# Performance work log

Hardware: AMD Instinct MI355X
Metric: run time of the kernel (lower is better)

## Reference

```python
import jax, jax.numpy as jnp
import numpy as np
import math

B, N, D, H = 1, 128, 256, 8
DK = D // H

def setup_inputs() -> dict:
    key = jax.random.key(0)
    ks = jax.random.split(key, 8)
    query = jax.random.normal(ks[0], (B, N, N, D), dtype=jnp.float32)
    key_t = jax.random.normal(ks[1], (B, N, N, D), dtype=jnp.float32)
    value = jax.random.normal(ks[2], (B, N, N, D), dtype=jnp.float32)
    mask = jax.random.randint(ks[3], (B, N, N, N), 0, 2).astype(jnp.bool_)
    s = 1.0 / math.sqrt(D)
    # torch nn.Linear weights: [out_features, in_features]
    Wk = jax.random.uniform(ks[4], (D, D), dtype=jnp.float32, minval=-s, maxval=s)
    Wv = jax.random.uniform(ks[5], (D, D), dtype=jnp.float32, minval=-s, maxval=s)
    Wq = jax.random.uniform(ks[6], (D, D), dtype=jnp.float32, minval=-s, maxval=s)
    Wo = jax.random.uniform(ks[7], (D, D), dtype=jnp.float32, minval=-s, maxval=s)
    return {"query": query, "key": key_t, "value": value, "mask": mask,
            "Wq": Wq, "Wk": Wk, "Wv": Wv, "Wo": Wo}

def reference(query, key, value, mask, Wq, Wk, Wv, Wo):
    b, n = query.shape[0], query.shape[1]
    # linear projections (no bias), then split heads -> [b, n, n, h, d_k]
    q = (query @ Wq.T).reshape(b, n, n, H, DK)
    k = (key @ Wk.T).reshape(b, n, n, H, DK)
    v = (value @ Wv.T).reshape(b, n, n, H, DK)
    scale = 1.0 / math.sqrt(DK)
    neg = jnp.float32(-1e9)
    m = mask[..., None]  # [b, n, n, n, 1] broadcast over heads
    # row attention: edge (x,y) attends over edges (x,z)
    scores_r = jnp.einsum('bxyhd,bxzhd->bxyzh', q, k) * scale
    scores_r = jnp.where(m, neg, scores_r)
    # column attention: edge (x,y) attends over edges (z,y)
    scores_l = jnp.einsum('bxyhd,bzyhd->bxyzh', q, k) * scale
    scores_l = jnp.where(m, neg, scores_l)
    scores = jnp.concatenate((scores_r, scores_l), axis=3)  # [b,n,n,2n,h]
    att = jax.nn.softmax(scores, axis=3)
    att_r, att_l = att[:, :, :, :n], att[:, :, :, n:]
    x_r = jnp.einsum('bxyzh,bxzhd->bxyhd', att_r, v)
    x_l = jnp.einsum('bxyzh,bzyhd->bxyhd', att_l, v)
    x = (x_r + x_l).reshape(b, n, n, D)
    return x @ Wo.T
```

## Files before the change

### kernel.cpp

```cpp
#include <hip/hip_runtime.h>
#include <hip/hip_bf16.h>
#include <math.h>

#define N_DIM 128
#define NH 8
#define DKH 32
#define M_ROWS (N_DIM * N_DIM)

typedef __attribute__((ext_vector_type(8))) short bf16x8;
typedef __attribute__((ext_vector_type(4))) float f32x4;

__device__ inline ushort f2b(float x) {
    union { __hip_bfloat16 b; ushort u; } c;
    c.b = __float2bfloat16(x);
    return c.u;
}

#define GLDS(src, dst) \
    __builtin_amdgcn_global_load_lds((const __attribute__((address_space(1))) void*)(src), \
                                     (__attribute__((address_space(3))) void*)(dst), 16, 0, 0)

__global__ __launch_bounds__(256) void cvt_w_kernel(const float* __restrict__ w0,
                                                    const float* __restrict__ w1,
                                                    const float* __restrict__ w2,
                                                    const float* __restrict__ w3,
                                                    ushort* __restrict__ out) {
    const int b = blockIdx.x;
    const int m = b >> 6;
    const float* src = (m == 0) ? w0 : (m == 1) ? w1 : (m == 2) ? w2 : w3;
    const int off = (b & 63) * 1024 + threadIdx.x * 4;
    float4 v = *(const float4*)(src + off);
    union { ushort u[4]; short4 s4; } p;
    p.u[0] = f2b(v.x); p.u[1] = f2b(v.y); p.u[2] = f2b(v.z); p.u[3] = f2b(v.w);
    *(short4*)(out + (size_t)m * 65536 + off) = p.s4;
}

template <bool ABF16, bool OBF16>
__global__ __launch_bounds__(512) void gemm_mfma(const void* __restrict__ Ain,
                                                 const ushort* __restrict__ Wb,
                                                 void* __restrict__ Cout) {
    __shared__ ushort As[2][64 * 32];
    __shared__ ushort Ws[2][256 * 32];
    const int tid = threadIdx.x;
    const int row0 = blockIdx.x * 64;
    const int w = tid >> 6, lane = tid & 63;
    const int lr = lane & 15, g = lane >> 4;
    const int wm = w & 3, wn = w >> 2;

    auto stage = [&](int t, int buf) {
        const int kbase = t * 32;
#pragma unroll
        for (int i = 0; i < 2; i++) {
            int c = i * 8 + w;
            const ushort* src = Wb + (size_t)(c * 16 + (lane >> 2)) * 256 + kbase + (lane & 3) * 8;
            GLDS(src, &Ws[buf][c * 512]);
        }
        if (ABF16) {
            if (tid < 256) {
                const ushort* Ab = (const ushort*)Ain;
                const ushort* src = Ab + (size_t)(row0 + w * 16 + (lane >> 2)) * 256 + kbase + (lane & 3) * 8;
                GLDS(src, &As[buf][w * 512]);
            }
        } else {
            const float* Af = (const float*)Ain;
            const int r = tid >> 3, k0 = (tid & 7) * 4;
            float4 v = *(const float4*)(Af + (size_t)(row0 + r) * 256 + kbase + k0);
            union { ushort u[4]; short4 s4; } p;
            p.u[0] = f2b(v.x); p.u[1] = f2b(v.y); p.u[2] = f2b(v.z); p.u[3] = f2b(v.w);
            *(short4*)&As[buf][r * 32 + k0] = p.s4;
        }
    };

    f32x4 acc[8];
    const f32x4 zero = {0.f, 0.f, 0.f, 0.f};
#pragma unroll
    for (int fc = 0; fc < 8; fc++) acc[fc] = zero;

    stage(0, 0);
    __syncthreads();

#pragma unroll
    for (int t = 0; t < 8; t++) {
        const int cur = t & 1;
        if (t < 7) stage(t + 1, cur ^ 1);
        bf16x8 aq = *(const bf16x8*)&As[cur][(wm * 16 + lr) * 32 + g * 8];
#pragma unroll
        for (int fc = 0; fc < 8; fc++) {
            bf16x8 bw = *(const bf16x8*)&Ws[cur][(wn * 128 + fc * 16 + lr) * 32 + g * 8];
            acc[fc] = __builtin_amdgcn_mfma_f32_16x16x32_bf16(aq, bw, acc[fc], 0, 0, 0);
        }
        __syncthreads();
    }

#pragma unroll
    for (int fc = 0; fc < 8; fc++) {
#pragma unroll
        for (int j = 0; j < 4; j++) {
            const int row = row0 + wm * 16 + g * 4 + j;
            const int col = wn * 128 + fc * 16 + lr;
            if (OBF16) ((ushort*)Cout)[(size_t)row * 256 + col] = f2b(acc[fc][j]);
            else       ((float*)Cout)[(size_t)row * 256 + col] = acc[fc][j];
        }
    }
}

template <int PASS>
__global__ __launch_bounds__(256) void attn_pass(const ushort* __restrict__ qb,
                                                 const ushort* __restrict__ kb,
                                                 const ushort* __restrict__ vb,
                                                 const int* __restrict__ mask,
                                                 float* __restrict__ ml,
                                                 float* __restrict__ sl,
                                                 float* __restrict__ Pl,
                                                 ushort* __restrict__ xb) {
    __shared__ ushort Qs[128 * 32];
    __shared__ ushort Ks[128 * 32];
    __shared__ ushort Vt[32 * 128];
    __shared__ ushort Ats[128 * 128];
    __shared__ float mlq[128], slq[128];

    const int tid = threadIdx.x;
    const int fixed = blockIdx.x >> 3;
    const int h = blockIdx.x & 7;

    int base, stride, mbase, mstride;
    if (PASS == 0) {
        base = (fixed * NH + h) * DKH;
        stride = N_DIM * NH * DKH;
        mbase = fixed * N_DIM;
        mstride = N_DIM * N_DIM;
    } else {
        base = fixed * N_DIM * NH * DKH + h * DKH;
        stride = NH * DKH;
        mbase = fixed * N_DIM * N_DIM;
        mstride = N_DIM;
    }

    if (PASS == 1) {
        if (tid < 128) mlq[tid] = ml[(tid * NH + h) * N_DIM + fixed];
        else           slq[tid - 128] = sl[((tid - 128) * NH + h) * N_DIM + fixed];
    }

#pragma unroll
    for (int i = 0; i < 2; i++) {
        int idx = tid + i * 256;
        int r = idx >> 2, d0 = (idx & 3) * 8;
        size_t goff = (size_t)base + (size_t)r * stride + d0;
        int4 qv = *(const int4*)(qb + goff);
        *(int4*)&Qs[r * 32 + d0] = qv;
        int4 kv = *(const int4*)(kb + goff);
        *(int4*)&Ks[r * 32 + d0] = kv;
        union { int4 v4; ushort u[8]; } uu;
        uu.v4 = *(const int4*)(vb + goff);
#pragma unroll
        for (int j = 0; j < 8; j++) {
            int d = d0 + j;
            int byte = d * 256 + r * 2;
            byte ^= (d & 7) << 4;
            Vt[byte >> 1] = uu.u[j];
        }
    }
    __syncthreads();

    const int w = tid >> 6;
    const int lane = tid & 63;
    const int lr = lane & 15;
    const int g = lane >> 4;
    const int rbase = w * 32;

    bf16x8 aq[2];
#pragma unroll
    for (int fr = 0; fr < 2; fr++)
        aq[fr] = *(const bf16x8*)&Qs[(rbase + fr * 16 + lr) * 32 + g * 8];

    f32x4 s[2][8];
    const f32x4 zero = {0.f, 0.f, 0.f, 0.f};
#pragma unroll
    for (int fc = 0; fc < 8; fc++) {
        bf16x8 bk = *(const bf16x8*)&Ks[(fc * 16 + lr) * 32 + g * 8];
#pragma unroll
        for (int fr = 0; fr < 2; fr++)
            s[fr][fc] = __builtin_amdgcn_mfma_f32_16x16x32_bf16(aq[fr], bk, zero, 0, 0, 0);
    }

    const float scale = 0.17677669529663687f;
    float mx[2][4], sm[2][4];
#pragma unroll
    for (int fr = 0; fr < 2; fr++) {
#pragma unroll
        for (int j = 0; j < 4; j++) {
            int row = rbase + fr * 16 + g * 4 + j;
            const int* mrow = mask + mbase + (size_t)row * mstride;
            float mmax = -3.0e38f;
#pragma unroll
            for (int fc = 0; fc < 8; fc++) {
                int col = fc * 16 + lr;
                float val = mrow[col] ? -1.0e9f : s[fr][fc][j] * scale;
                s[fr][fc][j] = val;
                mmax = fmaxf(mmax, val);
            }
            mmax = fmaxf(mmax, __shfl_xor(mmax, 1));
            mmax = fmaxf(mmax, __shfl_xor(mmax, 2));
            mmax = fmaxf(mmax, __shfl_xor(mmax, 4));
            mmax = fmaxf(mmax, __shfl_xor(mmax, 8));
            float ssum = 0.f;
#pragma unroll
            for (int fc = 0; fc < 8; fc++) {
                int col = fc * 16 + lr;
                float e = __expf(s[fr][fc][j] - mmax);
                ssum += e;
                int byte = row * 256 + col * 2;
                byte ^= (row & 7) << 4;
                Ats[byte >> 1] = f2b(e);
            }
            ssum += __shfl_xor(ssum, 1);
            ssum += __shfl_xor(ssum, 2);
            ssum += __shfl_xor(ssum, 4);
            ssum += __shfl_xor(ssum, 8);
            mx[fr][j] = mmax;
            sm[fr][j] = ssum;
        }
    }
    __syncthreads();

    f32x4 p[2][2];
    p[0][0] = zero; p[0][1] = zero; p[1][0] = zero; p[1][1] = zero;
#pragma unroll
    for (int ks = 0; ks < 4; ks++) {
        bf16x8 pa[2];
#pragma unroll
        for (int fr = 0; fr < 2; fr++) {
            int row = rbase + fr * 16 + lr;
            int byte = row * 256 + ks * 64 + g * 16;
            byte ^= (row & 7) << 4;
            pa[fr] = *(const bf16x8*)&Ats[byte >> 1];
        }
#pragma unroll
        for (int fc = 0; fc < 2; fc++) {
            int rd = fc * 16 + lr;
            int byte = rd * 256 + ks * 64 + g * 16;
            byte ^= (rd & 7) << 4;
            bf16x8 vbf = *(const bf16x8*)&Vt[byte >> 1];
#pragma unroll
            for (int fr = 0; fr < 2; fr++)
                p[fr][fc] = __builtin_amdgcn_mfma_f32_16x16x32_bf16(pa[fr], vbf, p[fr][fc], 0, 0, 0);
        }
    }

    if (PASS == 0) {
#pragma unroll
        for (int fr = 0; fr < 2; fr++) {
#pragma unroll
            for (int j = 0; j < 4; j++) {
                int row = rbase + fr * 16 + g * 4 + j;
                if (lr == 0) {
                    ml[(fixed * NH + h) * N_DIM + row] = mx[fr][j];
                    sl[(fixed * NH + h) * N_DIM + row] = sm[fr][j];
                }
#pragma unroll
                for (int fc = 0; fc < 2; fc++) {
                    int d = fc * 16 + lr;
                    Pl[((size_t)(fixed * NH + h) * N_DIM + row) * DKH + d] = p[fr][fc][j];
                }
            }
        }
    } else {
#pragma unroll
        for (int fr = 0; fr < 2; fr++) {
#pragma unroll
            for (int j = 0; j < 4; j++) {
                int row = rbase + fr * 16 + g * 4 + j;
                float mr = mx[fr][j], sr = sm[fr][j];
                float mlv = mlq[row], slv = slq[row];
                float m = fmaxf(mr, mlv);
                float cr = __expf(mr - m), cl = __expf(mlv - m);
                float inv = 1.0f / (sr * cr + slv * cl);
#pragma unroll
                for (int fc = 0; fc < 2; fc++) {
                    int d = fc * 16 + lr;
                    float plv = Pl[((size_t)(row * NH + h) * N_DIM + fixed) * DKH + d];
                    float o = (p[fr][fc][j] * cr + plv * cl) * inv;
                    xb[((size_t)fixed * N_DIM + row) * 256 + h * DKH + d] = f2b(o);
                }
            }
        }
    }
}

extern "C" void kernel_launch(void* const* d_in, const int* in_sizes, int n_in,
                              void* d_out, int out_size, void* d_ws, size_t ws_size,
                              hipStream_t stream) {
    const float* query = (const float*)d_in[0];
    const float* key_t = (const float*)d_in[1];
    const float* value = (const float*)d_in[2];
    const int*   mask  = (const int*)d_in[3];
    const float* Wq    = (const float*)d_in[4];
    const float* Wk    = (const float*)d_in[5];
    const float* Wv    = (const float*)d_in[6];
    const float* Wo    = (const float*)d_in[7];

    char* ws = (char*)d_ws;
    ushort* qb = (ushort*)ws;
    ushort* kb = (ushort*)(ws + (size_t)8 * 1024 * 1024);
    ushort* vb = (ushort*)(ws + (size_t)16 * 1024 * 1024);
    float*  ml = (float*)(ws + (size_t)24 * 1024 * 1024);
    float*  sl = (float*)(ws + (size_t)25 * 1024 * 1024);
    float*  Pl = (float*)(ws + (size_t)26 * 1024 * 1024);
    ushort* xb = (ushort*)(ws + (size_t)42 * 1024 * 1024);
    ushort* Wb = (ushort*)(ws + (size_t)50 * 1024 * 1024);

    cvt_w_kernel<<<256, 256, 0, stream>>>(Wq, Wk, Wv, Wo, Wb);
    gemm_mfma<false, true><<<M_ROWS / 64, 512, 0, stream>>>(query, Wb + 0 * 65536, qb);
    gemm_mfma<false, true><<<M_ROWS / 64, 512, 0, stream>>>(key_t, Wb + 1 * 65536, kb);
    gemm_mfma<false, true><<<M_ROWS / 64, 512, 0, stream>>>(value, Wb + 2 * 65536, vb);
    attn_pass<0><<<N_DIM * NH, 256, 0, stream>>>(qb, kb, vb, mask, ml, sl, Pl, xb);
    attn_pass<1><<<N_DIM * NH, 256, 0, stream>>>(qb, kb, vb, mask, ml, sl, Pl, xb);
    gemm_mfma<true, false><<<M_ROWS / 64, 512, 0, stream>>>(xb, Wb + 3 * 65536, (float*)d_out);
}
```

Baseline: 187.1 us.

## Batch QKV projections, pre-convert inputs to bf16, bit-pack mask, pad LDS

Adds a separate kernel that converts the three fp32 activation inputs to bf16 up front, so the GEMM can stage A with direct global-to-LDS loads. It replaces the projection GEMM with a batched 32-row-tile kernel that uses a K=64 step and XOR-swizzled LDS. The softmax scale is folded into the Q projection output. The attention kernels now ballot-pack each mask row into 128 bits in shared memory instead of reading ints per element, and pad the Q/K LDS rows to avoid bank conflicts. The trade-off is an extra full read and write pass over the activations for the conversion step.

```diff
diff --git a/kernel.cpp b/kernel.cpp
--- a/kernel.cpp
+++ b/kernel.cpp
@@ -35,73 +35,111 @@
     *(short4*)(out + (size_t)m * 65536 + off) = p.s4;
 }
 
-template <bool ABF16, bool OBF16>
-__global__ __launch_bounds__(512) void gemm_mfma(const void* __restrict__ Ain,
-                                                 const ushort* __restrict__ Wb,
-                                                 void* __restrict__ Cout) {
-    __shared__ ushort As[2][64 * 32];
-    __shared__ ushort Ws[2][256 * 32];
+__global__ __launch_bounds__(256) void cvt_a_kernel(const float* __restrict__ q,
+                                                    const float* __restrict__ k,
+                                                    const float* __restrict__ v,
+                                                    ushort* __restrict__ out) {
+    const int y = blockIdx.y;
+    const float* src = (y == 0) ? q : (y == 1) ? k : v;
+    const size_t base = ((size_t)blockIdx.x * 256 + threadIdx.x) * 8;
+    float4 a = *(const float4*)(src + base);
+    float4 b = *(const float4*)(src + base + 4);
+    union { ushort u[8]; int4 v4; } p;
+    p.u[0] = f2b(a.x); p.u[1] = f2b(a.y); p.u[2] = f2b(a.z); p.u[3] = f2b(a.w);
+    p.u[4] = f2b(b.x); p.u[5] = f2b(b.y); p.u[6] = f2b(b.z); p.u[7] = f2b(b.w);
+    *(int4*)(out + (size_t)y * (M_ROWS * 256) + base) = p.v4;
+}
+
+template <bool OBF16, bool BATCHED>
+__global__ __launch_bounds__(512) void gemm2(const ushort* __restrict__ Abase,
+                                             const ushort* __restrict__ Wbase,
+                                             void* __restrict__ Cbase,
+                                             float oscale0) {
+    __shared__ ushort As[2][32 * 64];
+    __shared__ ushort Ws[2][256 * 64];
     const int tid = threadIdx.x;
-    const int row0 = blockIdx.x * 64;
-    const int w = tid >> 6, lane = tid & 63;
-    const int lr = lane & 15, g = lane >> 4;
-    const int wm = w & 3, wn = w >> 2;
+    const int w = tid >> 6, l = tid & 63;
+    const int lr = l & 15, g = l >> 4;
+    const int row0 = blockIdx.x * 32;
+
+    const ushort* A = Abase;
+    const ushort* W = Wbase;
+    float oscale = oscale0;
+    size_t coff = 0;
+    if (BATCHED) {
+        const int y = blockIdx.y;
+        A += (size_t)y * (M_ROWS * 256);
+        W += (size_t)y * 65536;
+        coff = (size_t)y * (M_ROWS * 256);
+        oscale = (y == 0) ? oscale0 : 1.0f;
+    }
+
+    const int lrow = l >> 3;
+    const int kof = ((l & 7) ^ lrow) * 8;
 
     auto stage = [&](int t, int buf) {
-        const int kbase = t * 32;
-#pragma unroll
-        for (int i = 0; i < 2; i++) {
-            int c = i * 8 + w;
-            const ushort* src = Wb + (size_t)(c * 16 + (lane >> 2)) * 256 + kbase + (lane & 3) * 8;
-            GLDS(src, &Ws[buf][c * 512]);
-        }
-        if (ABF16) {
-            if (tid < 256) {
-                const ushort* Ab = (const ushort*)Ain;
-                const ushort* src = Ab + (size_t)(row0 + w * 16 + (lane >> 2)) * 256 + kbase + (lane & 3) * 8;
-                GLDS(src, &As[buf][w * 512]);
-            }
-        } else {
-            const float* Af = (const float*)Ain;
-            const int r = tid >> 3, k0 = (tid & 7) * 4;
-            float4 v = *(const float4*)(Af + (size_t)(row0 + r) * 256 + kbase + k0);
-            union { ushort u[4]; short4 s4; } p;
-            p.u[0] = f2b(v.x); p.u[1] = f2b(v.y); p.u[2] = f2b(v.z); p.u[3] = f2b(v.w);
-            *(short4*)&As[buf][r * 32 + k0] = p.s4;
+        const int kbase = t * 64;
+#pragma unroll
+        for (int i = 0; i < 4; i++) {
+            const int chunk = i * 8 + w;
+            GLDS(W + (size_t)(chunk * 8 + lrow) * 256 + kbase + kof,
+                 &Ws[buf][chunk * 512]);
+        }
+        if (w < 4) {
+            GLDS(A + (size_t)(row0 + w * 8 + lrow) * 256 + kbase + kof,
+                 &As[buf][w * 512]);
         }
     };
 
-    f32x4 acc[8];
+    f32x4 acc[2][2];
     const f32x4 zero = {0.f, 0.f, 0.f, 0.f};
-#pragma unroll
-    for (int fc = 0; fc < 8; fc++) acc[fc] = zero;
+    acc[0][0] = zero; acc[0][1] = zero; acc[1][0] = zero; acc[1][1] = zero;
 
     stage(0, 0);
     __syncthreads();
 
 #pragma unroll
-    for (int t = 0; t < 8; t++) {
+    for (int t = 0; t < 4; t++) {
         const int cur = t & 1;
-        if (t < 7) stage(t + 1, cur ^ 1);
-        bf16x8 aq = *(const bf16x8*)&As[cur][(wm * 16 + lr) * 32 + g * 8];
-#pragma unroll
-        for (int fc = 0; fc < 8; fc++) {
-            bf16x8 bw = *(const bf16x8*)&Ws[cur][(wn * 128 + fc * 16 + lr) * 32 + g * 8];
-            acc[fc] = __builtin_amdgcn_mfma_f32_16x16x32_bf16(aq, bw, acc[fc], 0, 0, 0);
+        if (t < 3) stage(t + 1, cur ^ 1);
+#pragma unroll
+        for (int kk = 0; kk < 2; kk++) {
+            bf16x8 a[2], b[2];
+#pragma unroll
+            for (int fr = 0; fr < 2; fr++) {
+                const int r = fr * 16 + lr;
+                int byte = r * 128 + kk * 64 + g * 16;
+                byte ^= (r & 7) << 4;
+                a[fr] = *(const bf16x8*)((const char*)&As[cur][0] + byte);
+            }
+#pragma unroll
+            for (int fc = 0; fc < 2; fc++) {
+                const int r = w * 32 + fc * 16 + lr;
+                int byte = r * 128 + kk * 64 + g * 16;
+                byte ^= (r & 7) << 4;
+                b[fc] = *(const bf16x8*)((const char*)&Ws[cur][0] + byte);
+            }
+#pragma unroll
+            for (int fr = 0; fr < 2; fr++)
+#pragma unroll
+                for (int fc = 0; fc < 2; fc++)
+                    acc[fr][fc] = __builtin_amdgcn_mfma_f32_16x16x32_bf16(a[fr], b[fc], acc[fr][fc], 0, 0, 0);
         }
         __syncthreads();
     }
 
 #pragma unroll
-    for (int fc = 0; fc < 8; fc++) {
-#pragma unroll
-        for (int j = 0; j < 4; j++) {
-            const int row = row0 + wm * 16 + g * 4 + j;
-            const int col = wn * 128 + fc * 16 + lr;
-            if (OBF16) ((ushort*)Cout)[(size_t)row * 256 + col] = f2b(acc[fc][j]);
-            else       ((float*)Cout)[(size_t)row * 256 + col] = acc[fc][j];
-        }
-    }
+    for (int fr = 0; fr < 2; fr++)
+#pragma unroll
+        for (int fc = 0; fc < 2; fc++)
+#pragma unroll
+            for (int j = 0; j < 4; j++) {
+                const int row = row0 + fr * 16 + g * 4 + j;
+                const int col = w * 32 + fc * 16 + lr;
+                const float vv = acc[fr][fc][j] * oscale;
+                if (OBF16) ((ushort*)Cbase)[coff + (size_t)row * 256 + col] = f2b(vv);
+                else       ((float*)Cbase)[(size_t)row * 256 + col] = vv;
+            }
 }
 
 template <int PASS>
@@ -113,10 +151,11 @@
                                                  float* __restrict__ sl,
                                                  float* __restrict__ Pl,
                                                  ushort* __restrict__ xb) {
-    __shared__ ushort Qs[128 * 32];
-    __shared__ ushort Ks[128 * 32];
+    __shared__ ushort Qs[128 * 40];
+    __shared__ ushort Ks[128 * 40];
     __shared__ ushort Vt[32 * 128];
     __shared__ ushort Ats[128 * 128];
+    __shared__ ulonglong2 Ms[128];
     __shared__ float mlq[128], slq[128];
 
     const int tid = threadIdx.x;
@@ -141,15 +180,26 @@
         else           slq[tid - 128] = sl[((tid - 128) * NH + h) * N_DIM + fixed];
     }
 
+    const int w = tid >> 6;
+    const int lane = tid & 63;
+
+    for (int rr = 0; rr < 32; rr++) {
+        const int row = w * 32 + rr;
+        const int* mrow = mask + mbase + (size_t)row * mstride;
+        unsigned long long lo = __ballot(mrow[lane] != 0);
+        unsigned long long hi = __ballot(mrow[64 + lane] != 0);
+        if (lane == 0) { Ms[row].x = lo; Ms[row].y = hi; }
+    }
+
 #pragma unroll
     for (int i = 0; i < 2; i++) {
         int idx = tid + i * 256;
         int r = idx >> 2, d0 = (idx & 3) * 8;
         size_t goff = (size_t)base + (size_t)r * stride + d0;
         int4 qv = *(const int4*)(qb + goff);
-        *(int4*)&Qs[r * 32 + d0] = qv;
+        *(int4*)&Qs[r * 40 + d0] = qv;
         int4 kv = *(const int4*)(kb + goff);
-        *(int4*)&Ks[r * 32 + d0] = kv;
+        *(int4*)&Ks[r * 40 + d0] = kv;
         union { int4 v4; ushort u[8]; } uu;
         uu.v4 = *(const int4*)(vb + goff);
 #pragma unroll
@@ -162,8 +212,6 @@
     }
     __syncthreads();
 
-    const int w = tid >> 6;
-    const int lane = tid & 63;
     const int lr = lane & 15;
     const int g = lane >> 4;
     const int rbase = w * 32;
@@ -171,31 +219,32 @@
     bf16x8 aq[2];
 #pragma unroll
     for (int fr = 0; fr < 2; fr++)
-        aq[fr] = *(const bf16x8*)&Qs[(rbase + fr * 16 + lr) * 32 + g * 8];
+        aq[fr] = *(const bf16x8*)&Qs[(rbase + fr * 16 + lr) * 40 + g * 8];
 
     f32x4 s[2][8];
     const f32x4 zero = {0.f, 0.f, 0.f, 0.f};
 #pragma unroll
     for (int fc = 0; fc < 8; fc++) {
-        bf16x8 bk = *(const bf16x8*)&Ks[(fc * 16 + lr) * 32 + g * 8];
+        bf16x8 bk = *(const bf16x8*)&Ks[(fc * 16 + lr) * 40 + g * 8];
 #pragma unroll
         for (int fr = 0; fr < 2; fr++)
             s[fr][fc] = __builtin_amdgcn_mfma_f32_16x16x32_bf16(aq[fr], bk, zero, 0, 0, 0);
     }
 
-    const float scale = 0.17677669529663687f;
     float mx[2][4], sm[2][4];
 #pragma unroll
     for (int fr = 0; fr < 2; fr++) {
 #pragma unroll
         for (int j = 0; j < 4; j++) {
-            int row = rbase + fr * 16 + g * 4 + j;
-            const int* mrow = mask + mbase + (size_t)row * mstride;
+            const int row = rbase + fr * 16 + g * 4 + j;
+            const ulonglong2 mb = Ms[row];
+            const unsigned long long mls = mb.x >> lr;
+            const unsigned long long mhs = mb.y >> lr;
             float mmax = -3.0e38f;
 #pragma unroll
             for (int fc = 0; fc < 8; fc++) {
-                int col = fc * 16 + lr;
-                float val = mrow[col] ? -1.0e9f : s[fr][fc][j] * scale;
+                const int bit = (int)(((fc < 4 ? mls : mhs) >> ((fc & 3) * 16)) & 1ull);
+                float val = bit ? -1.0e9f : s[fr][fc][j];
                 s[fr][fc][j] = val;
                 mmax = fmaxf(mmax, val);
             }
@@ -206,7 +255,7 @@
             float ssum = 0.f;
 #pragma unroll
             for (int fc = 0; fc < 8; fc++) {
-                int col = fc * 16 + lr;
+                const int col = fc * 16 + lr;
                 float e = __expf(s[fr][fc][j] - mmax);
                 ssum += e;
                 int byte = row * 256 + col * 2;
@@ -230,14 +279,14 @@
         bf16x8 pa[2];
 #pragma unroll
         for (int fr = 0; fr < 2; fr++) {
-            int row = rbase + fr * 16 + lr;
+            const int row = rbase + fr * 16 + lr;
             int byte = row * 256 + ks * 64 + g * 16;
             byte ^= (row & 7) << 4;
             pa[fr] = *(const bf16x8*)&Ats[byte >> 1];
         }
 #pragma unroll
         for (int fc = 0; fc < 2; fc++) {
-            int rd = fc * 16 + lr;
+            const int rd = fc * 16 + lr;
             int byte = rd * 256 + ks * 64 + g * 16;
             byte ^= (rd & 7) << 4;
             bf16x8 vbf = *(const bf16x8*)&Vt[byte >> 1];
@@ -252,14 +301,14 @@
         for (int fr = 0; fr < 2; fr++) {
 #pragma unroll
             for (int j = 0; j < 4; j++) {
-                int row = rbase + fr * 16 + g * 4 + j;
+                const int row = rbase + fr * 16 + g * 4 + j;
                 if (lr == 0) {
                     ml[(fixed * NH + h) * N_DIM + row] = mx[fr][j];
                     sl[(fixed * NH + h) * N_DIM + row] = sm[fr][j];
                 }
 #pragma unroll
                 for (int fc = 0; fc < 2; fc++) {
-                    int d = fc * 16 + lr;
+                    const int d = fc * 16 + lr;
                     Pl[((size_t)(fixed * NH + h) * N_DIM + row) * DKH + d] = p[fr][fc][j];
                 }
             }
@@ -269,17 +318,17 @@
         for (int fr = 0; fr < 2; fr++) {
 #pragma unroll
             for (int j = 0; j < 4; j++) {
-                int row = rbase + fr * 16 + g * 4 + j;
-                float mr = mx[fr][j], sr = sm[fr][j];
-                float mlv = mlq[row], slv = slq[row];
-                float m = fmaxf(mr, mlv);
-                float cr = __expf(mr - m), cl = __expf(mlv - m);
-                float inv = 1.0f / (sr * cr + slv * cl);
+                const int row = rbase + fr * 16 + g * 4 + j;
+                const float mr = mx[fr][j], sr = sm[fr][j];
+                const float mlv = mlq[row], slv = slq[row];
+                const float m = fmaxf(mr, mlv);
+                const float cr = __expf(mr - m), cl = __expf(mlv - m);
+                const float inv = 1.0f / (sr * cr + slv * cl);
 #pragma unroll
                 for (int fc = 0; fc < 2; fc++) {
-                    int d = fc * 16 + lr;
-                    float plv = Pl[((size_t)(row * NH + h) * N_DIM + fixed) * DKH + d];
-                    float o = (p[fr][fc][j] * cr + plv * cl) * inv;
+                    const int d = fc * 16 + lr;
+                    const float plv = Pl[((size_t)(row * NH + h) * N_DIM + fixed) * DKH + d];
+                    const float o = (p[fr][fc][j] * cr + plv * cl) * inv;
                     xb[((size_t)fixed * N_DIM + row) * 256 + h * DKH + d] = f2b(o);
                 }
             }
@@ -299,21 +348,24 @@
     const float* Wv    = (const float*)d_in[6];
     const float* Wo    = (const float*)d_in[7];
 
+    const size_t MB = 1024 * 1024;
     char* ws = (char*)d_ws;
-    ushort* qb = (ushort*)ws;
-    ushort* kb = (ushort*)(ws + (size_t)8 * 1024 * 1024);
-    ushort* vb = (ushort*)(ws + (size_t)16 * 1024 * 1024);
-    float*  ml = (float*)(ws + (size_t)24 * 1024 * 1024);
-    float*  sl = (float*)(ws + (size_t)25 * 1024 * 1024);
-    float*  Pl = (float*)(ws + (size_t)26 * 1024 * 1024);
-    ushort* xb = (ushort*)(ws + (size_t)42 * 1024 * 1024);
-    ushort* Wb = (ushort*)(ws + (size_t)50 * 1024 * 1024);
+    ushort* af = (ushort*)ws;
+    ushort* qb = (ushort*)(ws + 24 * MB);
+    ushort* kb = (ushort*)(ws + 32 * MB);
+    ushort* vb = (ushort*)(ws + 40 * MB);
+    ushort* xb = (ushort*)(ws + 48 * MB);
+    float*  Pl = (float*)(ws + 56 * MB);
+    float*  ml = (float*)(ws + 72 * MB);
+    float*  sl = (float*)(ws + 72 * MB + 512 * 1024);
+    ushort* Wb = (ushort*)(ws + 73 * MB);
+
+    const float qscale = 0.17677669529663687f;
 
     cvt_w_kernel<<<256, 256, 0, stream>>>(Wq, Wk, Wv, Wo, Wb);
-    gemm_mfma<false, true><<<M_ROWS / 64, 512, 0, stream>>>(query, Wb + 0 * 65536, qb);
-    gemm_mfma<false, true><<<M_ROWS / 64, 512, 0, stream>>>(key_t, Wb + 1 * 65536, kb);
-    gemm_mfma<false, true><<<M_ROWS / 64, 512, 0, stream>>>(value, Wb + 2 * 65536, vb);
+    cvt_a_kernel<<<dim3(2048, 3), 256, 0, stream>>>(query, key_t, value, af);
+    gemm2<true, true><<<dim3(M_ROWS / 32, 3), 512, 0, stream>>>(af, Wb, qb, qscale);
     attn_pass<0><<<N_DIM * NH, 256, 0, stream>>>(qb, kb, vb, mask, ml, sl, Pl, xb);
     attn_pass<1><<<N_DIM * NH, 256, 0, stream>>>(qb, kb, vb, mask, ml, sl, Pl, xb);
-    gemm_mfma<true, false><<<M_ROWS / 64, 512, 0, stream>>>(xb, Wb + 3 * 65536, (float*)d_out);
-}
+    gemm2<false, false><<<dim3(M_ROWS / 32, 1), 512, 0, stream>>>(xb, Wb + 3 * 65536, d_out, 1.0f);
+}
```

Measured after the change: 212.3 us. +13.5%, slower.
